# Kernel optimization log

Hardware: AMD Instinct MI355X
Metric: run time of the kernel (lower is better)

## Reference

```python
import jax, jax.numpy as jnp
import numpy as np

N, B, E = 2048, 2, 1024      # seq_len, batch, embedding_dims
H = 1024                      # hidden_dims
NH, D = 16, 64                # num_heads, head_dim (NH*D == H)
SCALE = 1.0 / float(np.sqrt(H))  # NOTE: module divides by sqrt(hidden_dims), not sqrt(head_dim)


def setup_inputs() -> dict:
    key = jax.random.key(0)
    k0, k1, k2 = jax.random.split(key, 3)
    x = jax.random.normal(k0, (N, B, E), dtype=jnp.float32)
    W_proj = jax.random.normal(k1, (E, 3 * H), dtype=jnp.float32) * 0.02
    b_proj = jnp.zeros((3 * H,), dtype=jnp.float32)
    W_out = jax.random.normal(k2, (H, E), dtype=jnp.float32) * 0.02
    b_out = jnp.zeros((E,), dtype=jnp.float32)
    return {"x": x, "W_proj": W_proj, "b_proj": b_proj, "W_out": W_out, "b_out": b_out}


def reference(x, W_proj, b_proj, W_out, b_out):
    n, b, _ = x.shape
    # QKV projection: [n, b, 3H] -> 'n b (k h d) -> k b h n d'
    proj = x @ W_proj + b_proj
    qkv = proj.reshape(n, b, 3, NH, D).transpose(2, 1, 3, 0, 4)  # [3, b, h, n, d]
    q, k, v = qkv[0], qkv[1], qkv[2]
    # scaled dot-product scores [b, h, n, n]
    scores = jnp.einsum('bhid,bhjd->bhij', q, k) * SCALE
    # causal mask: -inf above the diagonal (generate_square_subsequent_mask)
    i = jnp.arange(n)
    mask = jnp.where(i[None, :] > i[:, None], -jnp.inf, 0.0).astype(scores.dtype)
    att = jax.nn.softmax(scores + mask, axis=-1)  # dropout = identity (eval)
    out = jnp.einsum('bhij,bhjd->bhid', att, v)   # [b, h, n, d]
    out = out.transpose(2, 0, 1, 3).reshape(n, b, H)  # 'b h n d -> n b (h d)'
    return out @ W_out + b_out
```

## Files before the change

kernel.cpp:

```cpp
#include <hip/hip_runtime.h>
#include <cstdint>
#include <cstddef>

typedef __bf16 bf16_t;
typedef __bf16 bf16x8 __attribute__((ext_vector_type(8)));
typedef __bf16 bf16x4 __attribute__((ext_vector_type(4)));
typedef float f32x4 __attribute__((ext_vector_type(4)));

#define N_SEQ 2048
#define BATCH 2
#define EMB   1024
#define HID   1024
#define NHEAD 16
#define HDIM  64
#define NBROW (N_SEQ * BATCH)
#define ATT_SCALE2 (0.03125f * 1.44269504f)

#define EXP2F(x) __builtin_amdgcn_exp2f(x)

static __device__ __forceinline__ void async_copy16(const bf16_t* g, bf16_t* l) {
  __builtin_amdgcn_global_load_lds((const __attribute__((address_space(1))) void*)g,
                                   (__attribute__((address_space(3))) void*)l,
                                   16, 0, 0);
}

__global__ __launch_bounds__(256) void prep_kernel(
    const float* __restrict__ x, const float* __restrict__ Wp,
    const float* __restrict__ Wo, bf16_t* __restrict__ Xb,
    bf16_t* __restrict__ Wpt, bf16_t* __restrict__ Wot) {
  int bid = blockIdx.x;
  if (bid < 4096) {
    int i = (bid * 256 + threadIdx.x) * 4;
    float4 v = *(const float4*)(x + i);
    bf16x4 o;
    o[0] = (bf16_t)v.x; o[1] = (bf16_t)v.y; o[2] = (bf16_t)v.z; o[3] = (bf16_t)v.w;
    *(bf16x4*)(Xb + i) = o;
    return;
  }
  __shared__ float tile[32][33];
  const float* in; bf16_t* out; int R, C, bx;
  if (bid < 4096 + 3072) { bx = bid - 4096; in = Wp; out = Wpt; R = 1024; C = 3072; }
  else                   { bx = bid - 7168; in = Wo; out = Wot; R = 1024; C = 1024; }
  int gx = C / 32;
  int bc = (bx % gx) * 32, br = (bx / gx) * 32;
  int tx = threadIdx.x & 31, ty = threadIdx.x >> 5;
  #pragma unroll
  for (int i = 0; i < 32; i += 8)
    tile[ty + i][tx] = in[(size_t)(br + ty + i) * C + bc + tx];
  __syncthreads();
  #pragma unroll
  for (int i = 0; i < 32; i += 8)
    out[(size_t)(bc + ty + i) * R + br + tx] = (bf16_t)tile[tx][ty + i];
}

template <int BM, int BN, bool OUT_BF16, bool SCALEQ, bool WRITE_VT>
__global__ __launch_bounds__(256) void gemm_bt_kernel(
    const bf16_t* __restrict__ A, const bf16_t* __restrict__ Bt,
    const float* __restrict__ bias, void* __restrict__ Cout,
    bf16_t* __restrict__ Vt, int M, int Nn, int K) {
  constexpr int BK = 64;
  constexpr int MT = BM / 32;
  constexpr int NT = BN / 32;
  constexpr int CA = BM / 32;
  constexpr int CB = BN / 32;
  constexpr int ASZ = BM * BK;
  constexpr int BSZ = BN * BK;
  __shared__ __align__(16) bf16_t smem[2 * ASZ + 2 * BSZ];
  bf16_t* const Asb = smem;
  bf16_t* const Bsb = smem + 2 * ASZ;
  int tid = threadIdx.x;
  int wave = tid >> 6, lane = tid & 63;
  int c = lane & 15, quad = lane >> 4;
  int bm = blockIdx.x * BM;
  int bn = blockIdx.y * BN;
  int wm = (wave & 1) * (BM / 2), wn = (wave >> 1) * (BN / 2);
  f32x4 acc[MT][NT] = {};

  const bf16_t* agp[CA]; int alo[CA];
  const bf16_t* bgp[CB]; int blo[CB];
  #pragma unroll
  for (int i = 0; i < CA; ++i) {
    int p = i * 256 + tid;
    int row = p >> 3, ko = (p & 7) ^ (row & 7);
    agp[i] = A + (size_t)(bm + row) * K + ko * 8;
    alo[i] = (i * 256 + wave * 64) * 8;
  }
  #pragma unroll
  for (int i = 0; i < CB; ++i) {
    int p = i * 256 + tid;
    int row = p >> 3, ko = (p & 7) ^ (row & 7);
    bgp[i] = Bt + (size_t)(bn + row) * K + ko * 8;
    blo[i] = (i * 256 + wave * 64) * 8;
  }

  #pragma unroll
  for (int i = 0; i < CA; ++i) async_copy16(agp[i], Asb + alo[i]);
  #pragma unroll
  for (int i = 0; i < CB; ++i) async_copy16(bgp[i], Bsb + blo[i]);

  int nkb = K / BK;
  for (int ki = 0; ki < nkb; ++ki) {
    __syncthreads();
    if (ki + 1 < nkb) {
      int kb = (ki + 1) * BK;
      bf16_t* an = Asb + ((ki + 1) & 1) * ASZ;
      bf16_t* bnx = Bsb + ((ki + 1) & 1) * BSZ;
      #pragma unroll
      for (int i = 0; i < CA; ++i) async_copy16(agp[i] + kb, an + alo[i]);
      #pragma unroll
      for (int i = 0; i < CB; ++i) async_copy16(bgp[i] + kb, bnx + blo[i]);
    }
    const bf16_t* as = Asb + (ki & 1) * ASZ;
    const bf16_t* bs = Bsb + (ki & 1) * BSZ;
    #pragma unroll
    for (int kk = 0; kk < 2; ++kk) {
      bf16x8 af[MT], bf[NT];
      #pragma unroll
      for (int mt = 0; mt < MT; ++mt) {
        int row = wm + mt * 16 + c;
        int slot = (kk * 4 + quad) ^ (row & 7);
        af[mt] = *(const bf16x8*)(as + (size_t)(row * 8 + slot) * 8);
      }
      #pragma unroll
      for (int nt = 0; nt < NT; ++nt) {
        int row = wn + nt * 16 + c;
        int slot = (kk * 4 + quad) ^ (row & 7);
        bf[nt] = *(const bf16x8*)(bs + (size_t)(row * 8 + slot) * 8);
      }
      #pragma unroll
      for (int mt = 0; mt < MT; ++mt)
        #pragma unroll
        for (int nt = 0; nt < NT; ++nt)
          acc[mt][nt] = __builtin_amdgcn_mfma_f32_16x16x32_bf16(
              af[mt], bf[nt], acc[mt][nt], 0, 0, 0);
    }
  }

  bool do_vt = WRITE_VT && (bn >= 2 * HID);
  bf16_t* tb = smem;
  if (do_vt) __syncthreads();

  #pragma unroll
  for (int nt = 0; nt < NT; ++nt) {
    int col = bn + wn + nt * 16 + c;
    float bv = bias[col];
    float sc = (SCALEQ && col < HID) ? ATT_SCALE2 : 1.0f;
    #pragma unroll
    for (int mt = 0; mt < MT; ++mt) {
      #pragma unroll
      for (int r = 0; r < 4; ++r) {
        int loc = wm + mt * 16 + quad * 4 + r;
        int row = bm + loc;
        float v = (acc[mt][nt][r] + bv) * sc;
        if (OUT_BF16)
          ((bf16_t*)Cout)[(size_t)row * Nn + col] = (bf16_t)v;
        else
          ((float*)Cout)[(size_t)row * Nn + col] = v;
        if (do_vt) {
          int dg = wn + nt * 16 + c;
          int hh = dg >> 6, dl = dg & 63;
          tb[((loc & 1) * 2 + hh) * 4608 + dl * 72 + (loc >> 1)] = (bf16_t)v;
        }
      }
    }
  }

  if (do_vt) {
    __syncthreads();
    int h0 = (bn - 2 * HID) >> 6;
    int n2 = (tid & 7) * 8;
    #pragma unroll
    for (int i = 0; i < 2; ++i) {
      #pragma unroll
      for (int hh = 0; hh < 2; ++hh) {
        #pragma unroll
        for (int k = 0; k < 2; ++k) {
          int d = (tid >> 3) + k * 32;
          bf16x8 vv = *(const bf16x8*)(tb + ((i * 2 + hh) * 4608) + d * 72 + n2);
          *(bf16x8*)(Vt + (size_t)((i * 16 + h0 + hh) * HDIM + d) * N_SEQ + bm / 2 + n2) = vv;
        }
      }
    }
  }
}

__global__ __launch_bounds__(512, 4) void flash_attn_kernel(
    const bf16_t* __restrict__ Pj, const bf16_t* __restrict__ Vt,
    bf16_t* __restrict__ AO) {
  __shared__ __align__(16) bf16_t Ks[2][64 * 64];
  __shared__ __align__(16) bf16_t Vs[2][64 * 64];
  __shared__ __align__(16) bf16_t Ps[8][16 * 64];
  const int PJP = 3 * HID;
  int tid = threadIdx.x, wave = tid >> 6, lane = tid & 63;
  int c = lane & 15, quad = lane >> 4;
  int c7 = c & 7;
  int bid = blockIdx.x;
  int qb = (bid < 256) ? (15 - (bid >> 5)) : ((bid - 256) >> 5);
  int bh = bid & 31;
  int h = bh & 15, b = bh >> 4;
  int i0 = qb * 128;

  int i_row = i0 + wave * 16 + c;
  const bf16_t* qg = Pj + (size_t)(i_row * BATCH + b) * PJP + h * HDIM + quad * 8;
  bf16x8 qf0 = *(const bf16x8*)(qg);
  bf16x8 qf1 = *(const bf16x8*)(qg + 32);

  f32x4 o[4] = {};
  float lrow = 0.f;

  int jr = tid >> 3, oc = tid & 7;
  int lds_off = jr * 64 + (oc ^ (jr & 7)) * 8;
  const bf16_t* kg0 = Pj + (size_t)b * PJP + HID + h * HDIM + oc * 8;
  const bf16_t* vg0 = Vt + (size_t)(bh * HDIM + jr) * N_SEQ + oc * 8;

  int njt = 2 * qb + 2;
  bf16x8 kreg = *(const bf16x8*)(kg0 + (size_t)jr * BATCH * PJP);
  bf16x8 vreg = *(const bf16x8*)(vg0);

  for (int jt = 0; jt < njt; ++jt) {
    bf16_t* ks = Ks[jt & 1];
    bf16_t* vs = Vs[jt & 1];
    *(bf16x8*)(ks + lds_off) = kreg;
    *(bf16x8*)(vs + lds_off) = vreg;
    __syncthreads();
    if (jt + 1 < njt) {
      int j0n = (jt + 1) * 64;
      kreg = *(const bf16x8*)(kg0 + (size_t)(j0n + jr) * BATCH * PJP);
      vreg = *(const bf16x8*)(vg0 + j0n);
    }

    f32x4 st[4];
    #pragma unroll
    for (int mt = 0; mt < 4; ++mt) {
      const bf16_t* kr = ks + (mt * 16 + c) * 64;
      bf16x8 ka0 = *(const bf16x8*)(kr + ((quad) ^ c7) * 8);
      bf16x8 ka1 = *(const bf16x8*)(kr + ((quad + 4) ^ c7) * 8);
      f32x4 s = {};
      s = __builtin_amdgcn_mfma_f32_16x16x32_bf16(ka0, qf0, s, 0, 0, 0);
      st[mt] = __builtin_amdgcn_mfma_f32_16x16x32_bf16(ka1, qf1, s, 0, 0, 0);
    }
    if (jt >= 2 * qb) {
      int j0 = jt * 64;
      int ig = i0 + wave * 16 + c;
      #pragma unroll
      for (int mt = 0; mt < 4; ++mt)
        #pragma unroll
        for (int r = 0; r < 4; ++r)
          if (j0 + mt * 16 + quad * 4 + r > ig) st[mt][r] = -1e30f;
    }

    #pragma unroll
    for (int mt = 0; mt < 4; ++mt)
      #pragma unroll
      for (int r = 0; r < 4; ++r) {
        st[mt][r] = EXP2F(st[mt][r]);
        lrow += st[mt][r];
      }

    bf16_t* pw = Ps[wave];
    #pragma unroll
    for (int mt = 0; mt < 4; ++mt) {
      bf16x4 pv;
      #pragma unroll
      for (int r = 0; r < 4; ++r) pv[r] = (bf16_t)st[mt][r];
      int joct = mt * 2 + (quad >> 1);
      *(bf16x4*)(pw + c * 64 + (joct ^ c7) * 8 + (quad & 1) * 4) = pv;
    }
    const bf16_t* pr = pw + c * 64;
    bf16x8 pa0 = *(const bf16x8*)(pr + ((quad) ^ c7) * 8);
    bf16x8 pa1 = *(const bf16x8*)(pr + ((quad + 4) ^ c7) * 8);

    #pragma unroll
    for (int nt = 0; nt < 4; ++nt) {
      const bf16_t* vr = vs + (nt * 16 + c) * 64;
      bf16x8 vb0 = *(const bf16x8*)(vr + ((quad) ^ c7) * 8);
      bf16x8 vb1 = *(const bf16x8*)(vr + ((quad + 4) ^ c7) * 8);
      o[nt] = __builtin_amdgcn_mfma_f32_16x16x32_bf16(vb0, pa0, o[nt], 0, 0, 0);
      o[nt] = __builtin_amdgcn_mfma_f32_16x16x32_bf16(vb1, pa1, o[nt], 0, 0, 0);
    }
  }

  float lfull = lrow;
  lfull += __shfl_xor(lfull, 16);
  lfull += __shfl_xor(lfull, 32);
  float linv = 1.0f / lfull;
  int orow = (i0 + wave * 16 + c) * BATCH + b;
  #pragma unroll
  for (int nt = 0; nt < 4; ++nt) {
    bf16x4 pv;
    #pragma unroll
    for (int r = 0; r < 4; ++r) pv[r] = (bf16_t)(o[nt][r] * linv);
    *(bf16x4*)(AO + (size_t)orow * HID + h * HDIM + nt * 16 + quad * 4) = pv;
  }
}

extern "C" void kernel_launch(void* const* d_in, const int* in_sizes, int n_in,
                              void* d_out, int out_size, void* d_ws, size_t ws_size,
                              hipStream_t stream) {
  const float* x      = (const float*)d_in[0];
  const float* W_proj = (const float*)d_in[1];
  const float* b_proj = (const float*)d_in[2];
  const float* W_out  = (const float*)d_in[3];
  const float* b_out  = (const float*)d_in[4];

  bf16_t* Xb  = (bf16_t*)d_ws;
  bf16_t* Wpt = Xb  + (size_t)NBROW * EMB;
  bf16_t* Wot = Wpt + (size_t)3 * HID * EMB;
  bf16_t* Pj  = Wot + (size_t)HID * EMB;
  bf16_t* AO  = Pj  + (size_t)NBROW * 3 * HID;
  bf16_t* Vt  = AO  + (size_t)NBROW * HID;

  prep_kernel<<<8192, 256, 0, stream>>>(x, W_proj, W_out, Xb, Wpt, Wot);
  gemm_bt_kernel<128, 128, true, true, true>
      <<<dim3(NBROW / 128, 3 * HID / 128), 256, 0, stream>>>(
      Xb, Wpt, b_proj, (void*)Pj, Vt, NBROW, 3 * HID, EMB);
  flash_attn_kernel<<<512, 512, 0, stream>>>(Pj, Vt, AO);
  gemm_bt_kernel<128, 128, false, false, false>
      <<<dim3(NBROW / 128, EMB / 128), 256, 0, stream>>>(
      AO, Wot, b_out, d_out, nullptr, NBROW, EMB, HID);
}
```

Baseline: 160.8 us.

## Process two 16-row query tiles per wave in flash attention with 256 threads

The attention kernel now uses 4 waves per block instead of 8. Each wave handles 32 query rows, as two 16-row MFMA tiles that share every K and V fragment read from LDS. This halves LDS reads per unit of MFMA work. It also wraps the MFMA sections in s_setprio to favour matrix issue. The cost is more registers per wave (two sets of accumulators and scores) and fewer waves per block to hide latency, and each thread now loads two K/V chunks per tile.

Result: no change. 162.7 us (+1.2%).

```diff
diff --git a/kernel.cpp b/kernel.cpp
--- a/kernel.cpp
+++ b/kernel.cpp
@@ -184,7 +184,7 @@
   }
 }
 
-__global__ __launch_bounds__(512, 4) void flash_attn_kernel(
+__global__ __launch_bounds__(256, 3) void flash_attn_kernel(
     const bf16_t* __restrict__ Pj, const bf16_t* __restrict__ Vt,
     bf16_t* __restrict__ AO) {
   __shared__ __align__(16) bf16_t Ks[2][64 * 64];
@@ -200,97 +200,147 @@
   int h = bh & 15, b = bh >> 4;
   int i0 = qb * 128;
 
-  int i_row = i0 + wave * 16 + c;
-  const bf16_t* qg = Pj + (size_t)(i_row * BATCH + b) * PJP + h * HDIM + quad * 8;
-  bf16x8 qf0 = *(const bf16x8*)(qg);
-  bf16x8 qf1 = *(const bf16x8*)(qg + 32);
-
-  f32x4 o[4] = {};
-  float lrow = 0.f;
-
-  int jr = tid >> 3, oc = tid & 7;
-  int lds_off = jr * 64 + (oc ^ (jr & 7)) * 8;
+  bf16x8 qf00, qf01, qf10, qf11;
+  {
+    int ir0 = i0 + wave * 32 + c;
+    const bf16_t* qg0 = Pj + (size_t)(ir0 * BATCH + b) * PJP + h * HDIM + quad * 8;
+    qf00 = *(const bf16x8*)(qg0);
+    qf01 = *(const bf16x8*)(qg0 + 32);
+    const bf16_t* qg1 = qg0 + (size_t)16 * BATCH * PJP;
+    qf10 = *(const bf16x8*)(qg1);
+    qf11 = *(const bf16x8*)(qg1 + 32);
+  }
+
+  f32x4 o0[4] = {}, o1[4] = {};
+  float lrow0 = 0.f, lrow1 = 0.f;
+
+  int jr = tid >> 2, oc = tid & 3;
+  int so0 = (oc ^ (jr & 7)) * 8;
+  int so1 = ((oc + 4) ^ (jr & 7)) * 8;
+  int ldsrow = jr * 64;
   const bf16_t* kg0 = Pj + (size_t)b * PJP + HID + h * HDIM + oc * 8;
   const bf16_t* vg0 = Vt + (size_t)(bh * HDIM + jr) * N_SEQ + oc * 8;
 
   int njt = 2 * qb + 2;
-  bf16x8 kreg = *(const bf16x8*)(kg0 + (size_t)jr * BATCH * PJP);
-  bf16x8 vreg = *(const bf16x8*)(vg0);
+  bf16x8 kr0 = *(const bf16x8*)(kg0 + (size_t)jr * BATCH * PJP);
+  bf16x8 kr1 = *(const bf16x8*)(kg0 + (size_t)jr * BATCH * PJP + 32);
+  bf16x8 vr0 = *(const bf16x8*)(vg0);
+  bf16x8 vr1 = *(const bf16x8*)(vg0 + 32);
 
   for (int jt = 0; jt < njt; ++jt) {
     bf16_t* ks = Ks[jt & 1];
     bf16_t* vs = Vs[jt & 1];
-    *(bf16x8*)(ks + lds_off) = kreg;
-    *(bf16x8*)(vs + lds_off) = vreg;
+    *(bf16x8*)(ks + ldsrow + so0) = kr0;
+    *(bf16x8*)(ks + ldsrow + so1) = kr1;
+    *(bf16x8*)(vs + ldsrow + so0) = vr0;
+    *(bf16x8*)(vs + ldsrow + so1) = vr1;
     __syncthreads();
     if (jt + 1 < njt) {
       int j0n = (jt + 1) * 64;
-      kreg = *(const bf16x8*)(kg0 + (size_t)(j0n + jr) * BATCH * PJP);
-      vreg = *(const bf16x8*)(vg0 + j0n);
-    }
-
-    f32x4 st[4];
+      kr0 = *(const bf16x8*)(kg0 + (size_t)(j0n + jr) * BATCH * PJP);
+      kr1 = *(const bf16x8*)(kg0 + (size_t)(j0n + jr) * BATCH * PJP + 32);
+      vr0 = *(const bf16x8*)(vg0 + j0n);
+      vr1 = *(const bf16x8*)(vg0 + j0n + 32);
+    }
+
+    f32x4 st0[4], st1[4];
+    __builtin_amdgcn_s_setprio(1);
     #pragma unroll
     for (int mt = 0; mt < 4; ++mt) {
-      const bf16_t* kr = ks + (mt * 16 + c) * 64;
-      bf16x8 ka0 = *(const bf16x8*)(kr + ((quad) ^ c7) * 8);
-      bf16x8 ka1 = *(const bf16x8*)(kr + ((quad + 4) ^ c7) * 8);
-      f32x4 s = {};
-      s = __builtin_amdgcn_mfma_f32_16x16x32_bf16(ka0, qf0, s, 0, 0, 0);
-      st[mt] = __builtin_amdgcn_mfma_f32_16x16x32_bf16(ka1, qf1, s, 0, 0, 0);
-    }
+      const bf16_t* krp = ks + (mt * 16 + c) * 64;
+      bf16x8 ka0 = *(const bf16x8*)(krp + ((quad) ^ c7) * 8);
+      bf16x8 ka1 = *(const bf16x8*)(krp + ((quad + 4) ^ c7) * 8);
+      f32x4 s0 = {}, s1 = {};
+      s0 = __builtin_amdgcn_mfma_f32_16x16x32_bf16(ka0, qf00, s0, 0, 0, 0);
+      st0[mt] = __builtin_amdgcn_mfma_f32_16x16x32_bf16(ka1, qf01, s0, 0, 0, 0);
+      s1 = __builtin_amdgcn_mfma_f32_16x16x32_bf16(ka0, qf10, s1, 0, 0, 0);
+      st1[mt] = __builtin_amdgcn_mfma_f32_16x16x32_bf16(ka1, qf11, s1, 0, 0, 0);
+    }
+    __builtin_amdgcn_s_setprio(0);
+
     if (jt >= 2 * qb) {
       int j0 = jt * 64;
-      int ig = i0 + wave * 16 + c;
+      int ig0 = i0 + wave * 32 + c;
+      int ig1 = ig0 + 16;
       #pragma unroll
       for (int mt = 0; mt < 4; ++mt)
         #pragma unroll
-        for (int r = 0; r < 4; ++r)
-          if (j0 + mt * 16 + quad * 4 + r > ig) st[mt][r] = -1e30f;
+        for (int r = 0; r < 4; ++r) {
+          int jj = j0 + mt * 16 + quad * 4 + r;
+          if (jj > ig0) st0[mt][r] = -1e30f;
+          if (jj > ig1) st1[mt][r] = -1e30f;
+        }
     }
 
     #pragma unroll
     for (int mt = 0; mt < 4; ++mt)
       #pragma unroll
       for (int r = 0; r < 4; ++r) {
-        st[mt][r] = EXP2F(st[mt][r]);
-        lrow += st[mt][r];
-      }
-
-    bf16_t* pw = Ps[wave];
-    #pragma unroll
-    for (int mt = 0; mt < 4; ++mt) {
+        st0[mt][r] = EXP2F(st0[mt][r]);
+        lrow0 += st0[mt][r];
+        st1[mt][r] = EXP2F(st1[mt][r]);
+        lrow1 += st1[mt][r];
+      }
+
+    bf16x8 pa00, pa01, pa10, pa11;
+    {
+      bf16_t* pw = Ps[wave * 2];
+      #pragma unroll
+      for (int mt = 0; mt < 4; ++mt) {
+        bf16x4 pv;
+        #pragma unroll
+        for (int r = 0; r < 4; ++r) pv[r] = (bf16_t)st0[mt][r];
+        int joct = mt * 2 + (quad >> 1);
+        *(bf16x4*)(pw + c * 64 + (joct ^ c7) * 8 + (quad & 1) * 4) = pv;
+      }
+      const bf16_t* pr = pw + c * 64;
+      pa00 = *(const bf16x8*)(pr + ((quad) ^ c7) * 8);
+      pa01 = *(const bf16x8*)(pr + ((quad + 4) ^ c7) * 8);
+    }
+    {
+      bf16_t* pw = Ps[wave * 2 + 1];
+      #pragma unroll
+      for (int mt = 0; mt < 4; ++mt) {
+        bf16x4 pv;
+        #pragma unroll
+        for (int r = 0; r < 4; ++r) pv[r] = (bf16_t)st1[mt][r];
+        int joct = mt * 2 + (quad >> 1);
+        *(bf16x4*)(pw + c * 64 + (joct ^ c7) * 8 + (quad & 1) * 4) = pv;
+      }
+      const bf16_t* pr = pw + c * 64;
+      pa10 = *(const bf16x8*)(pr + ((quad) ^ c7) * 8);
+      pa11 = *(const bf16x8*)(pr + ((quad + 4) ^ c7) * 8);
+    }
+
+    __builtin_amdgcn_s_setprio(1);
+    #pragma unroll
+    for (int nt = 0; nt < 4; ++nt) {
+      const bf16_t* vrp = vs + (nt * 16 + c) * 64;
+      bf16x8 vb0 = *(const bf16x8*)(vrp + ((quad) ^ c7) * 8);
+      bf16x8 vb1 = *(const bf16x8*)(vrp + ((quad + 4) ^ c7) * 8);
+      o0[nt] = __builtin_amdgcn_mfma_f32_16x16x32_bf16(vb0, pa00, o0[nt], 0, 0, 0);
+      o0[nt] = __builtin_amdgcn_mfma_f32_16x16x32_bf16(vb1, pa01, o0[nt], 0, 0, 0);
+      o1[nt] = __builtin_amdgcn_mfma_f32_16x16x32_bf16(vb0, pa10, o1[nt], 0, 0, 0);
+      o1[nt] = __builtin_amdgcn_mfma_f32_16x16x32_bf16(vb1, pa11, o1[nt], 0, 0, 0);
+    }
+    __builtin_amdgcn_s_setprio(0);
+  }
+
+  #pragma unroll
+  for (int s = 0; s < 2; ++s) {
+    float lfull = s ? lrow1 : lrow0;
+    lfull += __shfl_xor(lfull, 16);
+    lfull += __shfl_xor(lfull, 32);
+    float linv = 1.0f / lfull;
+    int orow = (i0 + wave * 32 + s * 16 + c) * BATCH + b;
+    #pragma unroll
+    for (int nt = 0; nt < 4; ++nt) {
+      f32x4 ov = s ? o1[nt] : o0[nt];
       bf16x4 pv;
       #pragma unroll
-      for (int r = 0; r < 4; ++r) pv[r] = (bf16_t)st[mt][r];
-      int joct = mt * 2 + (quad >> 1);
-      *(bf16x4*)(pw + c * 64 + (joct ^ c7) * 8 + (quad & 1) * 4) = pv;
-    }
-    const bf16_t* pr = pw + c * 64;
-    bf16x8 pa0 = *(const bf16x8*)(pr + ((quad) ^ c7) * 8);
-    bf16x8 pa1 = *(const bf16x8*)(pr + ((quad + 4) ^ c7) * 8);
-
-    #pragma unroll
-    for (int nt = 0; nt < 4; ++nt) {
-      const bf16_t* vr = vs + (nt * 16 + c) * 64;
-      bf16x8 vb0 = *(const bf16x8*)(vr + ((quad) ^ c7) * 8);
-      bf16x8 vb1 = *(const bf16x8*)(vr + ((quad + 4) ^ c7) * 8);
-      o[nt] = __builtin_amdgcn_mfma_f32_16x16x32_bf16(vb0, pa0, o[nt], 0, 0, 0);
-      o[nt] = __builtin_amdgcn_mfma_f32_16x16x32_bf16(vb1, pa1, o[nt], 0, 0, 0);
-    }
-  }
-
-  float lfull = lrow;
-  lfull += __shfl_xor(lfull, 16);
-  lfull += __shfl_xor(lfull, 32);
-  float linv = 1.0f / lfull;
-  int orow = (i0 + wave * 16 + c) * BATCH + b;
-  #pragma unroll
-  for (int nt = 0; nt < 4; ++nt) {
-    bf16x4 pv;
-    #pragma unroll
-    for (int r = 0; r < 4; ++r) pv[r] = (bf16_t)(o[nt][r] * linv);
-    *(bf16x4*)(AO + (size_t)orow * HID + h * HDIM + nt * 16 + quad * 4) = pv;
+      for (int r = 0; r < 4; ++r) pv[r] = (bf16_t)(ov[r] * linv);
+      *(bf16x4*)(AO + (size_t)orow * HID + h * HDIM + nt * 16 + quad * 4) = pv;
+    }
   }
 }
 
@@ -314,7 +364,7 @@
   gemm_bt_kernel<128, 128, true, true, true>
       <<<dim3(NBROW / 128, 3 * HID / 128), 256, 0, stream>>>(
       Xb, Wpt, b_proj, (void*)Pj, Vt, NBROW, 3 * HID, EMB);
-  flash_attn_kernel<<<512, 512, 0, stream>>>(Pj, Vt, AO);
+  flash_attn_kernel<<<512, 256, 0, stream>>>(Pj, Vt, AO);
   gemm_bt_kernel<128, 128, false, false, false>
       <<<dim3(NBROW / 128, EMB / 128), 256, 0, stream>>>(
       AO, Wot, b_out, d_out, nullptr, NBROW, EMB, HID);
```

## Add 256x256 eight-wave QKV GEMM with four-stage async LDS pipeline

Applied to the files above, without the earlier changes.

Replaces the 128x128 QKV projection GEMM with a new 256x256-tile kernel using 8 waves, BK=32 stages and a 4-deep global_load_lds ring buffer with explicit vmcnt waits and raised MFMA priority. The larger tiles raise arithmetic intensity and the deeper pipeline is meant to hide global load latency. The V-transpose write is moved into the new kernel as a two-pass LDS staging step, and the old kernel's Vt path is removed. Risks: only 192 blocks on a large GPU (under one wave of CUs), higher register pressure with a 32-tile accumulator, and a 128KB shared buffer limiting occupancy.

Measured after the change: 164.3 us. 2.2% more time.

```diff
diff --git a/kernel.cpp b/kernel.cpp
--- a/kernel.cpp
+++ b/kernel.cpp
@@ -51,6 +51,146 @@
   #pragma unroll
   for (int i = 0; i < 32; i += 8)
     out[(size_t)(bc + ty + i) * R + br + tx] = (bf16_t)tile[tx][ty + i];
+}
+
+template <bool SCALEQ, bool WRITE_VT>
+__global__ __launch_bounds__(512, 2) void gemm8p_kernel(
+    const bf16_t* __restrict__ A, const bf16_t* __restrict__ Bt,
+    const float* __restrict__ bias, bf16_t* __restrict__ Cout,
+    bf16_t* __restrict__ Vt, int Nn, int K) {
+  constexpr int BM = 256, BN = 256;
+  __shared__ __align__(16) bf16_t sm[4 * 16384];
+  int tid = threadIdx.x;
+  int wave = tid >> 6, lane = tid & 63;
+  int c = lane & 15, quad = lane >> 4;
+  int bm = blockIdx.x * BM, bn = blockIdx.y * BN;
+  int wm = (wave >> 2) * 128;
+  int wn = (wave & 3) * 64;
+
+  f32x4 acc[8][4] = {};
+
+  const bf16_t* agp[2]; const bf16_t* bgp[2]; int aldo[2];
+  #pragma unroll
+  for (int i = 0; i < 2; ++i) {
+    int p = i * 512 + tid;
+    int row = p >> 2;
+    int ko = (p & 3) ^ ((row >> 1) & 3);
+    agp[i] = A + (size_t)(bm + row) * K + ko * 8;
+    bgp[i] = Bt + (size_t)(bn + row) * K + ko * 8;
+    aldo[i] = (i * 512 + wave * 64) * 8;
+  }
+
+  auto stage = [&](int s) {
+    int q = s & 3, ks = s * 32;
+    bf16_t* ab = sm + q * 16384;
+    bf16_t* bb = ab + 8192;
+    #pragma unroll
+    for (int i = 0; i < 2; ++i) {
+      async_copy16(agp[i] + ks, ab + aldo[i]);
+      async_copy16(bgp[i] + ks, bb + aldo[i]);
+    }
+  };
+
+  auto compute = [&](int s) {
+    int q = s & 3;
+    const bf16_t* ab = sm + q * 16384;
+    const bf16_t* bb = ab + 8192;
+    bf16x8 af[8], bfr[4];
+    #pragma unroll
+    for (int mt = 0; mt < 8; ++mt) {
+      int row = wm + mt * 16 + c;
+      int slot = (quad ^ (row >> 1)) & 3;
+      af[mt] = *(const bf16x8*)(ab + row * 32 + slot * 8);
+    }
+    #pragma unroll
+    for (int nt = 0; nt < 4; ++nt) {
+      int row = wn + nt * 16 + c;
+      int slot = (quad ^ (row >> 1)) & 3;
+      bfr[nt] = *(const bf16x8*)(bb + row * 32 + slot * 8);
+    }
+    __builtin_amdgcn_s_setprio(1);
+    #pragma unroll
+    for (int mt = 0; mt < 8; ++mt)
+      #pragma unroll
+      for (int nt = 0; nt < 4; ++nt)
+        acc[mt][nt] = __builtin_amdgcn_mfma_f32_16x16x32_bf16(
+            af[mt], bfr[nt], acc[mt][nt], 0, 0, 0);
+    __builtin_amdgcn_s_setprio(0);
+  };
+
+  int nHK = K / 32;
+  stage(0); stage(1); stage(2);
+  for (int s = 0; s < nHK - 3; ++s) {
+    asm volatile("s_waitcnt vmcnt(8)" ::: "memory");
+    __builtin_amdgcn_s_barrier();
+    asm volatile("" ::: "memory");
+    stage(s + 3);
+    compute(s);
+  }
+  asm volatile("s_waitcnt vmcnt(8)" ::: "memory");
+  __builtin_amdgcn_s_barrier();
+  asm volatile("" ::: "memory");
+  compute(nHK - 3);
+  asm volatile("s_waitcnt vmcnt(4)" ::: "memory");
+  __builtin_amdgcn_s_barrier();
+  asm volatile("" ::: "memory");
+  compute(nHK - 2);
+  asm volatile("s_waitcnt vmcnt(0)" ::: "memory");
+  __builtin_amdgcn_s_barrier();
+  asm volatile("" ::: "memory");
+  compute(nHK - 1);
+
+  #pragma unroll
+  for (int nt = 0; nt < 4; ++nt) {
+    int col = bn + wn + nt * 16 + c;
+    float bv = bias[col];
+    float sc = (SCALEQ && col < HID) ? ATT_SCALE2 : 1.0f;
+    #pragma unroll
+    for (int mt = 0; mt < 8; ++mt)
+      #pragma unroll
+      for (int r = 0; r < 4; ++r) {
+        int loc = wm + mt * 16 + quad * 4 + r;
+        float v = (acc[mt][nt][r] + bv) * sc;
+        Cout[(size_t)(bm + loc) * Nn + col] = (bf16_t)v;
+      }
+  }
+
+  if (WRITE_VT && (bn >= 2 * HID)) {
+    int h0 = (bn - 2 * HID) >> 6;
+    #pragma unroll
+    for (int pass = 0; pass < 2; ++pass) {
+      asm volatile("" ::: "memory");
+      __builtin_amdgcn_s_barrier();
+      asm volatile("" ::: "memory");
+      #pragma unroll
+      for (int nt = 0; nt < 4; ++nt) {
+        int dg = wn + nt * 16 + c;
+        int hh = dg >> 6, dl = dg & 63;
+        float bv = bias[bn + dg];
+        #pragma unroll
+        for (int mt = 0; mt < 8; ++mt)
+          #pragma unroll
+          for (int r = 0; r < 4; ++r) {
+            int loc = wm + mt * 16 + quad * 4 + r;
+            if ((loc & 1) == pass)
+              sm[hh * 8704 + dl * 136 + (loc >> 1)] = (bf16_t)(acc[mt][nt][r] + bv);
+          }
+      }
+      asm volatile("" ::: "memory");
+      __builtin_amdgcn_s_barrier();
+      asm volatile("" ::: "memory");
+      #pragma unroll
+      for (int j = 0; j < 8; ++j) {
+        int idx = j * 512 + tid;
+        int nv = idx & 15;
+        int d = (idx >> 4) & 63;
+        int hh = idx >> 10;
+        bf16x8 vv = *(const bf16x8*)(sm + hh * 8704 + d * 136 + nv * 8);
+        *(bf16x8*)(Vt + (size_t)((pass * 16 + h0 + hh) * HDIM + d) * N_SEQ
+                   + bm / 2 + nv * 8) = vv;
+      }
+    }
+  }
 }
 
 template <int BM, int BN, bool OUT_BF16, bool SCALEQ, bool WRITE_VT>
@@ -136,10 +276,6 @@
     }
   }
 
-  bool do_vt = WRITE_VT && (bn >= 2 * HID);
-  bf16_t* tb = smem;
-  if (do_vt) __syncthreads();
-
   #pragma unroll
   for (int nt = 0; nt < NT; ++nt) {
     int col = bn + wn + nt * 16 + c;
@@ -156,29 +292,6 @@
           ((bf16_t*)Cout)[(size_t)row * Nn + col] = (bf16_t)v;
         else
           ((float*)Cout)[(size_t)row * Nn + col] = v;
-        if (do_vt) {
-          int dg = wn + nt * 16 + c;
-          int hh = dg >> 6, dl = dg & 63;
-          tb[((loc & 1) * 2 + hh) * 4608 + dl * 72 + (loc >> 1)] = (bf16_t)v;
-        }
-      }
-    }
-  }
-
-  if (do_vt) {
-    __syncthreads();
-    int h0 = (bn - 2 * HID) >> 6;
-    int n2 = (tid & 7) * 8;
-    #pragma unroll
-    for (int i = 0; i < 2; ++i) {
-      #pragma unroll
-      for (int hh = 0; hh < 2; ++hh) {
-        #pragma unroll
-        for (int k = 0; k < 2; ++k) {
-          int d = (tid >> 3) + k * 32;
-          bf16x8 vv = *(const bf16x8*)(tb + ((i * 2 + hh) * 4608) + d * 72 + n2);
-          *(bf16x8*)(Vt + (size_t)((i * 16 + h0 + hh) * HDIM + d) * N_SEQ + bm / 2 + n2) = vv;
-        }
       }
     }
   }
@@ -311,9 +424,9 @@
   bf16_t* Vt  = AO  + (size_t)NBROW * HID;
 
   prep_kernel<<<8192, 256, 0, stream>>>(x, W_proj, W_out, Xb, Wpt, Wot);
-  gemm_bt_kernel<128, 128, true, true, true>
-      <<<dim3(NBROW / 128, 3 * HID / 128), 256, 0, stream>>>(
-      Xb, Wpt, b_proj, (void*)Pj, Vt, NBROW, 3 * HID, EMB);
+  gemm8p_kernel<true, true>
+      <<<dim3(NBROW / 256, 3 * HID / 256), 512, 0, stream>>>(
+      Xb, Wpt, b_proj, Pj, Vt, 3 * HID, EMB);
   flash_attn_kernel<<<512, 512, 0, stream>>>(Pj, Vt, AO);
   gemm_bt_kernel<128, 128, false, false, false>
       <<<dim3(NBROW / 128, EMB / 128), 256, 0, stream>>>(
```

## Split long causal query blocks across two workgroups and combine partial results

Applied to the files above, without the earlier changes.

The upper half of the query blocks, which have the longest causal key ranges, are now each split into two key-range parts handled by separate workgroups. These write unnormalized fp32 partial outputs and row sums to workspace, and a new combine kernel adds them and normalizes. The aim is to balance work across the grid and reduce the tail from the heaviest blocks. The cost is an extra launch and extra fp32 memory traffic. Partials are summed without a max rescale, which relies on the kernel's existing fixed-offset softmax form.

Result: slower. 168.5 us (+4.8%).

```diff
diff --git a/kernel.cpp b/kernel.cpp
--- a/kernel.cpp
+++ b/kernel.cpp
@@ -186,7 +186,7 @@
 
 __global__ __launch_bounds__(512, 4) void flash_attn_kernel(
     const bf16_t* __restrict__ Pj, const bf16_t* __restrict__ Vt,
-    bf16_t* __restrict__ AO) {
+    bf16_t* __restrict__ AO, float* __restrict__ OP, float* __restrict__ Lp) {
   __shared__ __align__(16) bf16_t Ks[2][64 * 64];
   __shared__ __align__(16) bf16_t Vs[2][64 * 64];
   __shared__ __align__(16) bf16_t Ps[8][16 * 64];
@@ -195,8 +195,24 @@
   int c = lane & 15, quad = lane >> 4;
   int c7 = c & 7;
   int bid = blockIdx.x;
-  int qb = (bid < 256) ? (15 - (bid >> 5)) : ((bid - 256) >> 5);
-  int bh = bid & 31;
+
+  int qb, part, bh, jt0, jt1;
+  bool heavy;
+  if (bid < 512) {
+    heavy = true;
+    qb = 15 - (bid >> 6);
+    part = (bid >> 5) & 1;
+    bh = bid & 31;
+    jt0 = part ? (qb + 1) : 0;
+    jt1 = part ? (2 * qb + 2) : (qb + 1);
+  } else {
+    heavy = false;
+    qb = 7 - ((bid - 512) >> 5);
+    part = 0;
+    bh = (bid - 512) & 31;
+    jt0 = 0;
+    jt1 = 2 * qb + 2;
+  }
   int h = bh & 15, b = bh >> 4;
   int i0 = qb * 128;
 
@@ -213,17 +229,16 @@
   const bf16_t* kg0 = Pj + (size_t)b * PJP + HID + h * HDIM + oc * 8;
   const bf16_t* vg0 = Vt + (size_t)(bh * HDIM + jr) * N_SEQ + oc * 8;
 
-  int njt = 2 * qb + 2;
-  bf16x8 kreg = *(const bf16x8*)(kg0 + (size_t)jr * BATCH * PJP);
-  bf16x8 vreg = *(const bf16x8*)(vg0);
-
-  for (int jt = 0; jt < njt; ++jt) {
+  bf16x8 kreg = *(const bf16x8*)(kg0 + (size_t)(jt0 * 64 + jr) * BATCH * PJP);
+  bf16x8 vreg = *(const bf16x8*)(vg0 + jt0 * 64);
+
+  for (int jt = jt0; jt < jt1; ++jt) {
     bf16_t* ks = Ks[jt & 1];
     bf16_t* vs = Vs[jt & 1];
     *(bf16x8*)(ks + lds_off) = kreg;
     *(bf16x8*)(vs + lds_off) = vreg;
     __syncthreads();
-    if (jt + 1 < njt) {
+    if (jt + 1 < jt1) {
       int j0n = (jt + 1) * 64;
       kreg = *(const bf16x8*)(kg0 + (size_t)(j0n + jr) * BATCH * PJP);
       vreg = *(const bf16x8*)(vg0 + j0n);
@@ -283,15 +298,43 @@
   float lfull = lrow;
   lfull += __shfl_xor(lfull, 16);
   lfull += __shfl_xor(lfull, 32);
-  float linv = 1.0f / lfull;
   int orow = (i0 + wave * 16 + c) * BATCH + b;
-  #pragma unroll
-  for (int nt = 0; nt < 4; ++nt) {
-    bf16x4 pv;
-    #pragma unroll
-    for (int r = 0; r < 4; ++r) pv[r] = (bf16_t)(o[nt][r] * linv);
-    *(bf16x4*)(AO + (size_t)orow * HID + h * HDIM + nt * 16 + quad * 4) = pv;
-  }
+
+  if (!heavy) {
+    float linv = 1.0f / lfull;
+    #pragma unroll
+    for (int nt = 0; nt < 4; ++nt) {
+      bf16x4 pv;
+      #pragma unroll
+      for (int r = 0; r < 4; ++r) pv[r] = (bf16_t)(o[nt][r] * linv);
+      *(bf16x4*)(AO + (size_t)orow * HID + h * HDIM + nt * 16 + quad * 4) = pv;
+    }
+  } else {
+    float* op = OP + (size_t)part * NBROW * HID + (size_t)orow * HID + h * HDIM;
+    #pragma unroll
+    for (int nt = 0; nt < 4; ++nt)
+      *(f32x4*)(op + nt * 16 + quad * 4) = o[nt];
+    if (lane < 16)
+      Lp[part * 32 * N_SEQ + bh * N_SEQ + (i0 + wave * 16 + c)] = lfull;
+  }
+}
+
+__global__ __launch_bounds__(256) void combine_kernel(
+    const float* __restrict__ OP, const float* __restrict__ Lp,
+    bf16_t* __restrict__ AO) {
+  int gid = blockIdx.x * 256 + threadIdx.x;
+  int col = (gid & 255) * 4;
+  int row = 2048 + (gid >> 8);
+  int i = row >> 1, b = row & 1;
+  int bh = b * 16 + (col >> 6);
+  f32x4 a = *(const f32x4*)(OP + (size_t)row * HID + col);
+  f32x4 c2 = *(const f32x4*)(OP + (size_t)NBROW * HID + (size_t)row * HID + col);
+  float l = Lp[bh * N_SEQ + i] + Lp[32 * N_SEQ + bh * N_SEQ + i];
+  float rinv = 1.0f / l;
+  bf16x4 o;
+  #pragma unroll
+  for (int r = 0; r < 4; ++r) o[r] = (bf16_t)((a[r] + c2[r]) * rinv);
+  *(bf16x4*)(AO + (size_t)row * HID + col) = o;
 }
 
 extern "C" void kernel_launch(void* const* d_in, const int* in_sizes, int n_in,
@@ -309,12 +352,15 @@
   bf16_t* Pj  = Wot + (size_t)HID * EMB;
   bf16_t* AO  = Pj  + (size_t)NBROW * 3 * HID;
   bf16_t* Vt  = AO  + (size_t)NBROW * HID;
+  float*  OP  = (float*)(Vt + (size_t)32 * HDIM * N_SEQ);
+  float*  Lp  = OP + (size_t)2 * NBROW * HID;
 
   prep_kernel<<<8192, 256, 0, stream>>>(x, W_proj, W_out, Xb, Wpt, Wot);
   gemm_bt_kernel<128, 128, true, true, true>
       <<<dim3(NBROW / 128, 3 * HID / 128), 256, 0, stream>>>(
       Xb, Wpt, b_proj, (void*)Pj, Vt, NBROW, 3 * HID, EMB);
-  flash_attn_kernel<<<512, 512, 0, stream>>>(Pj, Vt, AO);
+  flash_attn_kernel<<<768, 512, 0, stream>>>(Pj, Vt, AO, OP, Lp);
+  combine_kernel<<<2048, 256, 0, stream>>>(OP, Lp, AO);
   gemm_bt_kernel<128, 128, false, false, false>
       <<<dim3(NBROW / 128, EMB / 128), 256, 0, stream>>>(
       AO, Wot, b_out, d_out, nullptr, NBROW, EMB, HID);
```
